# Kernel tuning notes

Hardware: AMD Instinct MI355X
Metric: run time of the kernel (lower is better)

Reference implementation:

```python
import jax, jax.numpy as jnp
import numpy as np

BS, NCAM, N, S = 2, 3, 64, 256


def setup_inputs() -> dict:
    key = jax.random.key(0)
    ks = jax.random.split(key, 7)
    # 2D projected points in pixel coordinates [0, image_size)
    points = jax.random.uniform(ks[0], (BS, NCAM, N, 2), dtype=jnp.float32) * S
    # blob params (per-point), realistic trained-model ranges
    sigmas = jax.random.uniform(ks[1], (BS, N), dtype=jnp.float32) * 0.05 + 0.02
    exponents = jax.random.uniform(ks[2], (BS, N), dtype=jnp.float32) * 0.5 + 0.75
    intensities = jax.random.uniform(ks[3], (BS, N), dtype=jnp.float32) * 0.5 + 0.5
    # per-camera scale factors, near 1
    camera_sigmas = jax.random.uniform(ks[4], (BS, NCAM), dtype=jnp.float32) * 0.2 + 0.9
    camera_exponents = jax.random.uniform(ks[5], (BS, NCAM), dtype=jnp.float32) * 0.2 + 0.9
    camera_intensities = jax.random.uniform(ks[6], (BS, NCAM), dtype=jnp.float32) * 0.2 + 0.9
    return {
        "points": points,
        "sigmas": sigmas,
        "exponents": exponents,
        "intensities": intensities,
        "camera_sigmas": camera_sigmas,
        "camera_exponents": camera_exponents,
        "camera_intensities": camera_intensities,
        "image_size": S,
    }


def reference(points, sigmas, exponents, intensities,
              camera_sigmas, camera_exponents, camera_intensities, image_size):
    """Faithful JAX port of render_points (render_mode='gaussians')."""
    bs, ncam, n = points.shape[0], points.shape[1], points.shape[2]
    s2 = image_size // 2
    # normalize pixel coords to [-1, 1] and flatten batch*cameras
    p = jnp.clip((points - s2) / s2, -1.0, 1.0).reshape(bs * ncam, n, 2)
    # per-point params scaled by per-camera factors; repeat_interleave(3,0)
    # on (bs,N) == broadcast over camera axis then flatten -> (bs*3, N, 1, 1)
    sig = (sigmas[:, None, :] * camera_sigmas[:, :, None]).reshape(bs * ncam, n, 1, 1)
    expn = (exponents[:, None, :] * camera_exponents[:, :, None]).reshape(bs * ncam, n, 1, 1)
    inten = (intensities[:, None, :] * camera_intensities[:, :, None]).reshape(bs * ncam, n, 1, 1)
    grid = jnp.linspace(-1.0, 1.0, image_size, dtype=jnp.float32)
    # m[y, x] = (grid[x], grid[y]); squared distance to each point
    dx = grid[None, None, None, :] - p[:, :, 0, None, None]   # (bs*3, N, 1, W)
    dy = grid[None, None, :, None] - p[:, :, 1, None, None]   # (bs*3, N, H, 1)
    dst = dx * dx + dy * dy                                   # (bs*3, N, H, W)
    blobs = jnp.exp(-((dst / (2.0 * sig * sig)) ** expn))      # (bs*3, N, H, W)
    masks = jnp.minimum(jnp.max(blobs * inten, axis=1), 1.0)   # amax over N, clamp(max=1)
    masks = masks.reshape(bs, ncam, image_size, image_size)
    blobs = blobs.reshape(bs, ncam, n, image_size, image_size)
    return masks, blobs
```

## Files before the change

kernel.cpp:

```cpp
#include <hip/hip_runtime.h>

constexpr int S_IMG = 256;
constexpr int NPT   = 64;
constexpr int BC    = 6;
constexpr int NCAM_ = 3;

typedef float vf2 __attribute__((ext_vector_type(2)));

__device__ __forceinline__ float blob_eval(float u, float e) {
    float v = exp2f(e * __log2f(u));
    return exp2f(-1.4426950408889634f * v);
}

__global__ __launch_bounds__(256) void render_fused(
    const float* __restrict__ points,
    const float* __restrict__ sigmas,
    const float* __restrict__ exponents,
    const float* __restrict__ intensities,
    const float* __restrict__ cam_sig,
    const float* __restrict__ cam_exp,
    const float* __restrict__ cam_int,
    float* __restrict__ masks,
    float* __restrict__ blobs)
{
    const int blk = blockIdx.x;
    const int bc  = blk >> 7;
    const int y0  = (blk & 127) << 1;
    const int b   = bc / NCAM_;
    const int t   = threadIdx.x;

    __shared__ float spx[NPT], spy[NPT], sk[NPT], se[NPT], si[NPT], srn[NPT];
    if (t < NPT) {
        float px = points[(bc * NPT + t) * 2 + 0];
        float py = points[(bc * NPT + t) * 2 + 1];
        px = fminf(fmaxf((px - 128.0f) * (1.0f / 128.0f), -1.0f), 1.0f);
        py = fminf(fmaxf((py - 128.0f) * (1.0f / 128.0f), -1.0f), 1.0f);
        float sg = sigmas[b * NPT + t] * cam_sig[bc];
        float e  = exponents[b * NPT + t] * cam_exp[bc];
        spx[t] = px;
        spy[t] = py;
        sk[t]  = 1.0f / (2.0f * sg * sg);
        se[t]  = e;
        si[t]  = intensities[b * NPT + t] * cam_int[bc];
        srn[t] = exp2f(3.2034f / e);
    }
    __syncthreads();

    const int lin = t << 1;
    const int y   = y0 + (lin >> 8);
    const int x   = lin & 255;

    const float step = 2.0f / 255.0f;
    const float gx0  = fmaf((float)x, step, -1.0f);
    const float gx1  = gx0 + step;
    const float gy   = fmaf((float)y, step, -1.0f);

    float m0 = 0.0f, m1 = 0.0f;
    float* bp = blobs + ((size_t)bc * NPT << 16) + ((size_t)y << 8) + x;
    const size_t nstride = (size_t)S_IMG * S_IMG;

    #pragma unroll 4
    for (int n = 0; n < NPT; ++n) {
        float kk   = sk[n];
        float dx0  = gx0 - spx[n];
        float dx1  = gx1 - spx[n];
        float dyv  = gy  - spy[n];
        float kdy2 = kk * dyv * dyv;
        float u0   = fmaf(kk * dx0, dx0, kdy2);
        float u1   = fmaf(kk * dx1, dx1, kdy2);
        float rn   = srn[n];
        vf2 o; o.x = 0.0f; o.y = 0.0f;
        if (fminf(u0, u1) < rn) {
            float e  = se[n];
            float it = si[n];
            if (u0 < rn) {
                o.x = blob_eval(u0, e);
                m0  = fmaxf(m0, o.x * it);
            }
            if (u1 < rn) {
                o.y = blob_eval(u1, e);
                m1  = fmaxf(m1, o.y * it);
            }
        }
        *reinterpret_cast<vf2*>(bp + n * nstride) = o;
    }

    vf2 mm;
    mm.x = fminf(m0, 1.0f);
    mm.y = fminf(m1, 1.0f);
    *reinterpret_cast<vf2*>(masks + ((size_t)bc << 16)
                                  + ((size_t)y << 8) + x) = mm;
}

extern "C" void kernel_launch(void* const* d_in, const int* in_sizes, int n_in,
                              void* d_out, int out_size, void* d_ws, size_t ws_size,
                              hipStream_t stream) {
    const float* points      = (const float*)d_in[0];
    const float* sigmas      = (const float*)d_in[1];
    const float* exponents   = (const float*)d_in[2];
    const float* intensities = (const float*)d_in[3];
    const float* cam_sig     = (const float*)d_in[4];
    const float* cam_exp     = (const float*)d_in[5];
    const float* cam_int     = (const float*)d_in[6];

    float* masks = (float*)d_out;
    float* blobs = (float*)d_out + (size_t)BC * S_IMG * S_IMG;

    dim3 grid(BC * (S_IMG / 2));
    dim3 block(256);
    render_fused<<<grid, block, 0, stream>>>(
        points, sigmas, exponents, intensities, cam_sig, cam_exp, cam_int,
        masks, blobs);
}
```

Before: 21.56 us.

## Pack per-point params into vector LDS records and use one-row blocks

Per-point parameters move from six separate shared arrays into one float4 and one float2 record, so each point needs fewer LDS reads. The grid changes to one image row per 128-thread block, which doubles the block count. The per-pixel cutoff branches are merged: once either pixel passes, both pixels are evaluated. This is safe because exp(-u^e) underflows to zero beyond the cutoff. The change trades some extra transcendental work for less divergence and fewer LDS instructions.

New measurement: 21.56 us. Within noise of the previous version (+0.0%).

```diff
diff --git a/kernel.cpp b/kernel.cpp
--- a/kernel.cpp
+++ b/kernel.cpp
@@ -6,13 +6,14 @@
 constexpr int NCAM_ = 3;
 
 typedef float vf2 __attribute__((ext_vector_type(2)));
+typedef float vf4 __attribute__((ext_vector_type(4)));
 
 __device__ __forceinline__ float blob_eval(float u, float e) {
     float v = exp2f(e * __log2f(u));
     return exp2f(-1.4426950408889634f * v);
 }
 
-__global__ __launch_bounds__(256) void render_fused(
+__global__ __launch_bounds__(128) void render_fused(
     const float* __restrict__ points,
     const float* __restrict__ sigmas,
     const float* __restrict__ exponents,
@@ -24,12 +25,13 @@
     float* __restrict__ blobs)
 {
     const int blk = blockIdx.x;
-    const int bc  = blk >> 7;
-    const int y0  = (blk & 127) << 1;
+    const int bc  = blk >> 8;
+    const int y   = blk & 255;
     const int b   = bc / NCAM_;
     const int t   = threadIdx.x;
 
-    __shared__ float spx[NPT], spy[NPT], sk[NPT], se[NPT], si[NPT], srn[NPT];
+    __shared__ vf4 sP[NPT];
+    __shared__ vf2 sQ[NPT];
     if (t < NPT) {
         float px = points[(bc * NPT + t) * 2 + 0];
         float py = points[(bc * NPT + t) * 2 + 1];
@@ -37,18 +39,20 @@
         py = fminf(fmaxf((py - 128.0f) * (1.0f / 128.0f), -1.0f), 1.0f);
         float sg = sigmas[b * NPT + t] * cam_sig[bc];
         float e  = exponents[b * NPT + t] * cam_exp[bc];
-        spx[t] = px;
-        spy[t] = py;
-        sk[t]  = 1.0f / (2.0f * sg * sg);
-        se[t]  = e;
-        si[t]  = intensities[b * NPT + t] * cam_int[bc];
-        srn[t] = exp2f(3.2034f / e);
+        vf4 P;
+        P.x = px;
+        P.y = py;
+        P.z = 1.0f / (2.0f * sg * sg);
+        P.w = exp2f(3.2034f / e);
+        sP[t] = P;
+        vf2 Q;
+        Q.x = e;
+        Q.y = intensities[b * NPT + t] * cam_int[bc];
+        sQ[t] = Q;
     }
     __syncthreads();
 
-    const int lin = t << 1;
-    const int y   = y0 + (lin >> 8);
-    const int x   = lin & 255;
+    const int x = t << 1;
 
     const float step = 2.0f / 255.0f;
     const float gx0  = fmaf((float)x, step, -1.0f);
@@ -61,26 +65,20 @@
 
     #pragma unroll 4
     for (int n = 0; n < NPT; ++n) {
-        float kk   = sk[n];
-        float dx0  = gx0 - spx[n];
-        float dx1  = gx1 - spx[n];
-        float dyv  = gy  - spy[n];
-        float kdy2 = kk * dyv * dyv;
-        float u0   = fmaf(kk * dx0, dx0, kdy2);
-        float u1   = fmaf(kk * dx1, dx1, kdy2);
-        float rn   = srn[n];
+        vf4 P = sP[n];
+        float dx0  = gx0 - P.x;
+        float dx1  = gx1 - P.x;
+        float dyv  = gy  - P.y;
+        float kdy2 = P.z * dyv * dyv;
+        float u0   = fmaf(P.z * dx0, dx0, kdy2);
+        float u1   = fmaf(P.z * dx1, dx1, kdy2);
         vf2 o; o.x = 0.0f; o.y = 0.0f;
-        if (fminf(u0, u1) < rn) {
-            float e  = se[n];
-            float it = si[n];
-            if (u0 < rn) {
-                o.x = blob_eval(u0, e);
-                m0  = fmaxf(m0, o.x * it);
-            }
-            if (u1 < rn) {
-                o.y = blob_eval(u1, e);
-                m1  = fmaxf(m1, o.y * it);
-            }
+        if (fminf(u0, u1) < P.w) {
+            vf2 Q = sQ[n];
+            o.x = blob_eval(u0, Q.x);
+            o.y = blob_eval(u1, Q.x);
+            m0 = fmaxf(m0, o.x * Q.y);
+            m1 = fmaxf(m1, o.y * Q.y);
         }
         *reinterpret_cast<vf2*>(bp + n * nstride) = o;
     }
@@ -106,8 +104,8 @@
     float* masks = (float*)d_out;
     float* blobs = (float*)d_out + (size_t)BC * S_IMG * S_IMG;
 
-    dim3 grid(BC * (S_IMG / 2));
-    dim3 block(256);
+    dim3 grid(BC * S_IMG);
+    dim3 block(128);
     render_fused<<<grid, block, 0, stream>>>(
         points, sigmas, exponents, intensities, cam_sig, cam_exp, cam_int,
         masks, blobs);
```
